# Kernel optimization log

Measured on AMD Instinct MI355X. Metric: run time of the kernel, lower is better.

The kernel has to match this reference:

```python
import jax, jax.numpy as jnp
import numpy as np

EPS = 1e-6
N_LATENT = 64
LITTLE_LATENT = 16
PATCH = 5
N_PATCH_SIDE = 21           # (63+2-5)/3+1
N_PATCHES = N_PATCH_SIDE ** 2  # 441
DEC_SIDE = 13               # decoder fold uses 13x13 = 169 tiles


def _make_patch_kernel():
    # Faithful to create_kernel(): eps-filled kernel with identity taps, grouped per color channel.
    k = np.full((25, 25), EPS, dtype=np.float32)
    k[np.arange(25), np.arange(25)] += 1.0
    k = k.reshape(25, 1, PATCH, PATCH)
    return jnp.asarray(np.tile(k, (3, 1, 1, 1)))  # (75, 1, 5, 5), OIHW


def extract_image_patches(x):
    # x: [B, 3, 63, 63] -> [B, 441, 3, 5, 5]
    kern = _make_patch_kernel().astype(x.dtype)
    out = jax.lax.conv_general_dilated(
        x, kern, window_strides=(3, 3), padding=((1, 1), (1, 1)),
        feature_group_count=3, dimension_numbers=('NCHW', 'OIHW', 'NCHW'))  # [B, 75, 21, 21]
    B = x.shape[0]
    out = out.reshape(B, 3, PATCH, PATCH, N_PATCHES)
    return out.transpose(0, 4, 1, 2, 3)


def little_encode(p_flat, le_w1, le_b1, le_w2, le_b2):
    # p_flat: [N, 75] -> mean, logvar each [N, 16]
    h = jax.nn.relu(p_flat @ le_w1 + le_b1)
    stats = h @ le_w2 + le_b2
    return stats[:, :LITTLE_LATENT], stats[:, LITTLE_LATENT:]


def little_decode(z, ld_w1, ld_b1, ld_w2, ld_b2):
    # z: [N, 16] -> [N, 3, 5, 5]
    h = jax.nn.relu(z @ ld_w1 + ld_b1)
    out = jax.nn.sigmoid(h @ ld_w2 + ld_b2)
    return out.reshape(-1, 3, PATCH, PATCH)


def setup_inputs() -> dict:
    key = jax.random.key(0)
    ks = jax.random.split(key, 20)
    B = 256
    s = 0.02  # weight init scale for numerical sanity
    inp = {
        'x': jax.random.uniform(ks[0], (B, 3, 63, 63), jnp.float32),
        'noise_little': jax.random.normal(ks[1], (B, N_PATCHES, LITTLE_LATENT), jnp.float32),
        'noise_z': jax.random.normal(ks[2], (B, N_LATENT), jnp.float32),
        # little VAE params (LittleVAE_V2([3,5,5],16), MLP stand-in)
        'le_w1': jax.random.normal(ks[3], (75, 128), jnp.float32) * s,
        'le_b1': jnp.zeros((128,), jnp.float32),
        'le_w2': jax.random.normal(ks[4], (128, 2 * LITTLE_LATENT), jnp.float32) * s,
        'le_b2': jnp.zeros((2 * LITTLE_LATENT,), jnp.float32),
        'ld_w1': jax.random.normal(ks[5], (LITTLE_LATENT, 128), jnp.float32) * s,
        'ld_b1': jnp.zeros((128,), jnp.float32),
        'ld_w2': jax.random.normal(ks[6], (128, 75), jnp.float32) * s,
        'ld_b2': jnp.zeros((75,), jnp.float32),
        # encoder_mlp: Linear(7056,4096) ReLU Linear(4096,2*n_latent) ReLU
        'enc_w1': jax.random.normal(ks[7], (7056, 4096), jnp.float32) * s,
        'enc_b1': jnp.zeros((4096,), jnp.float32),
        'enc_w2': jax.random.normal(ks[8], (4096, 2 * N_LATENT), jnp.float32) * s,
        'enc_b2': jnp.zeros((2 * N_LATENT,), jnp.float32),
        # decoder_mlp: Linear(n_latent,32) ReLU Linear(32,4096) ReLU Linear(4096,7056) ReLU
        'dec_w1': jax.random.normal(ks[9], (N_LATENT, 32), jnp.float32) * s,
        'dec_b1': jnp.zeros((32,), jnp.float32),
        'dec_w2': jax.random.normal(ks[10], (32, 4096), jnp.float32) * s,
        'dec_b2': jnp.zeros((4096,), jnp.float32),
        'dec_w3': jax.random.normal(ks[11], (4096, 7056), jnp.float32) * s,
        'dec_b3': jnp.zeros((7056,), jnp.float32),
    }
    return inp


def reference(x, noise_little, noise_z,
              le_w1, le_b1, le_w2, le_b2, ld_w1, ld_b1, ld_w2, ld_b2,
              enc_w1, enc_b1, enc_w2, enc_b2,
              dec_w1, dec_b1, dec_w2, dec_b2, dec_w3, dec_b3):
    B = x.shape[0]
    patches = extract_image_patches(x)                      # [B, 441, 3, 5, 5]
    p_flat = patches.reshape(B * N_PATCHES, 75)
    m_l, lv_l = little_encode(p_flat, le_w1, le_b1, le_w2, le_b2)  # [B*441, 16]
    z_l = noise_little.reshape(B * N_PATCHES, LITTLE_LATENT) * jnp.exp(0.5 * lv_l) + m_l
    next_layer_input = z_l.reshape(B, N_PATCHES, 1, LITTLE_LATENT)

    # hierarchical encode (note trailing ReLU applies to mean/logvar, as in source)
    h = jax.nn.relu(next_layer_input.reshape(B, -1) @ enc_w1 + enc_b1)
    stats = jax.nn.relu(h @ enc_w2 + enc_b2)
    mean, logvar = stats[:, :N_LATENT], stats[:, N_LATENT:]
    z = noise_z * jnp.exp(0.5 * logvar) + mean

    # hierarchical decode
    h = jax.nn.relu(z @ dec_w1 + dec_b1)
    h = jax.nn.relu(h @ dec_w2 + dec_b2)
    latent = jax.nn.relu(h @ dec_w3 + dec_b3).reshape(B, N_PATCHES, 1, LITTLE_LATENT)

    # fold first 169 decoded 5x5 tiles (stride 5 => non-overlapping) into 65x65, crop to 64x64
    z_tiles = latent[:, :DEC_SIDE * DEC_SIDE, 0, :].reshape(B * DEC_SIDE * DEC_SIDE, LITTLE_LATENT)
    tiles = little_decode(z_tiles, ld_w1, ld_b1, ld_w2, ld_b2)  # [B*169, 3, 5, 5]
    tiles = tiles.reshape(B, DEC_SIDE, DEC_SIDE, 3, PATCH, PATCH)
    canvas = tiles.transpose(0, 3, 1, 4, 2, 5).reshape(B, 3, DEC_SIDE * PATCH, DEC_SIDE * PATCH)
    img = canvas[:, :, :-1, :-1]                             # [B, 3, 64, 64]
    return (latent, mean, logvar, next_layer_input, img)
```

## Files before the change

### kernel.cpp

```cpp
#include <hip/hip_runtime.h>
#include <math.h>

#define EPSF 1e-6f

typedef __attribute__((ext_vector_type(8))) short short8v;
typedef __attribute__((ext_vector_type(4))) float f32x4;
typedef __attribute__((ext_vector_type(4))) unsigned short u16x4;

__device__ __forceinline__ unsigned short f2bf(float f) {
    union { float f; unsigned u; } v; v.f = f;
    return (unsigned short)((v.u + 0x7FFFu + ((v.u >> 16) & 1u)) >> 16);
}
__device__ __forceinline__ int swe(int row, int k) {
    return (row << 7) + (k ^ ((row & 7) << 3));
}
__device__ __forceinline__ int swe64(int row, int k) {
    return (row << 6) + (k ^ ((row & 7) << 3));
}

__global__ __launch_bounds__(256) void k_little_encode_mfma(
    const float* __restrict__ x,
    const float* __restrict__ noise,
    const float* __restrict__ w1,
    const float* __restrict__ b1,
    const float* __restrict__ w2,
    const float* __restrict__ b2,
    float* __restrict__ nli,
    unsigned short* __restrict__ nli_bf)
{
    __shared__ __align__(16) unsigned short pS[128 * 128];
    __shared__ __align__(16) unsigned short w1S[128 * 128];
    __shared__ __align__(16) unsigned short hS[128 * 128];
    __shared__ __align__(16) unsigned short w2S[32 * 128];
    __shared__ float b1S[128];
    __shared__ float b2S[32];
    __shared__ float sums[128][4];

    int t = threadIdx.x;

    {
        uint4 z4 = make_uint4(0, 0, 0, 0);
        #pragma unroll
        for (int i = 0; i < 8; ++i) {
            *(uint4*)&pS[(i * 256 + t) * 8]  = z4;
            *(uint4*)&w1S[(i * 256 + t) * 8] = z4;
        }
    }
    __syncthreads();

    for (int k = (t >> 4); k < 75; k += 16) {
        int n0 = (t & 15) * 8;
        float4 a0 = *(const float4*)(w1 + k * 128 + n0);
        float4 a1 = *(const float4*)(w1 + k * 128 + n0 + 4);
        w1S[swe(n0 + 0, k)] = f2bf(a0.x);
        w1S[swe(n0 + 1, k)] = f2bf(a0.y);
        w1S[swe(n0 + 2, k)] = f2bf(a0.z);
        w1S[swe(n0 + 3, k)] = f2bf(a0.w);
        w1S[swe(n0 + 4, k)] = f2bf(a1.x);
        w1S[swe(n0 + 5, k)] = f2bf(a1.y);
        w1S[swe(n0 + 6, k)] = f2bf(a1.z);
        w1S[swe(n0 + 7, k)] = f2bf(a1.w);
    }
    for (int k = (t >> 3); k < 128; k += 32) {
        int n0 = (t & 7) * 4;
        float4 a = *(const float4*)(w2 + k * 32 + n0);
        w2S[swe(n0 + 0, k)] = f2bf(a.x);
        w2S[swe(n0 + 1, k)] = f2bf(a.y);
        w2S[swe(n0 + 2, k)] = f2bf(a.z);
        w2S[swe(n0 + 3, k)] = f2bf(a.w);
    }
    if (t < 128) b1S[t] = b1[t];
    if (t < 32)  b2S[t] = b2[t];

    int row  = t & 127;
    int half = t >> 7;
    int R0 = blockIdx.x * 128 + row;
    int bb = R0 / 441;
    int p  = R0 - bb * 441;
    int pi = p / 21, pj = p - pi * 21;
    const float* xb = x + (size_t)bb * 3 * 63 * 63;

    float v[38];
    {
        float sA = 0.f, sB = 0.f;
        if (half == 0) {
            #pragma unroll
            for (int i = 0; i < 38; ++i) {
                const int k = i;
                const int c = k / 25, o = k % 25, ph = o / 5, pw = o % 5;
                int y = pi * 3 + ph - 1, xx = pj * 3 + pw - 1;
                float val = 0.f;
                if ((unsigned)y < 63u && (unsigned)xx < 63u)
                    val = xb[(c * 63 + y) * 63 + xx];
                v[i] = val;
                if (k < 25) sA += val; else sB += val;
            }
        } else {
            #pragma unroll
            for (int i = 0; i < 37; ++i) {
                const int k = 38 + i;
                const int c = k / 25, o = k % 25, ph = o / 5, pw = o % 5;
                int y = pi * 3 + ph - 1, xx = pj * 3 + pw - 1;
                float val = 0.f;
                if ((unsigned)y < 63u && (unsigned)xx < 63u)
                    val = xb[(c * 63 + y) * 63 + xx];
                v[i] = val;
                if (k < 50) sA += val; else sB += val;
            }
        }
        sums[row][half * 2 + 0] = sA;
        sums[row][half * 2 + 1] = sB;
    }
    __syncthreads();
    {
        float c0 = sums[row][0];
        float c1 = sums[row][1] + sums[row][2];
        float c2 = sums[row][3];
        if (half == 0) {
            #pragma unroll
            for (int i = 0; i < 38; ++i) {
                const int k = i;
                float cs = (k < 25) ? c0 : c1;
                pS[swe(row, k)] = f2bf(v[i] + EPSF * cs);
            }
        } else {
            #pragma unroll
            for (int i = 0; i < 37; ++i) {
                const int k = 38 + i;
                float cs = (k < 50) ? c1 : c2;
                pS[swe(row, k)] = f2bf(v[i] + EPSF * cs);
            }
        }
    }
    __syncthreads();

    int w = t >> 6, lane = t & 63, lr = lane & 15, lg = lane >> 4;

    f32x4 acc[2][8];
    #pragma unroll
    for (int mi = 0; mi < 2; ++mi)
        #pragma unroll
        for (int ni = 0; ni < 8; ++ni)
            acc[mi][ni] = (f32x4){0.f, 0.f, 0.f, 0.f};

    #pragma unroll
    for (int ks = 0; ks < 3; ++ks) {
        int kb = ks * 32 + lg * 8;
        short8v a0 = *(const short8v*)&pS[swe(w * 32 + lr, kb)];
        short8v a1 = *(const short8v*)&pS[swe(w * 32 + 16 + lr, kb)];
        #pragma unroll
        for (int ni = 0; ni < 8; ++ni) {
            short8v bf = *(const short8v*)&w1S[swe(ni * 16 + lr, kb)];
            acc[0][ni] = __builtin_amdgcn_mfma_f32_16x16x32_bf16(a0, bf, acc[0][ni], 0, 0, 0);
            acc[1][ni] = __builtin_amdgcn_mfma_f32_16x16x32_bf16(a1, bf, acc[1][ni], 0, 0, 0);
        }
    }
    #pragma unroll
    for (int mi = 0; mi < 2; ++mi)
        #pragma unroll
        for (int ni = 0; ni < 8; ++ni) {
            int n = ni * 16 + lr;
            float bv = b1S[n];
            #pragma unroll
            for (int r = 0; r < 4; ++r) {
                int m = w * 32 + mi * 16 + lg * 4 + r;
                hS[swe(m, n)] = f2bf(fmaxf(acc[mi][ni][r] + bv, 0.f));
            }
        }

    f32x4 acc2[2][2];
    #pragma unroll
    for (int mi = 0; mi < 2; ++mi)
        #pragma unroll
        for (int ni = 0; ni < 2; ++ni)
            acc2[mi][ni] = (f32x4){0.f, 0.f, 0.f, 0.f};

    #pragma unroll
    for (int kh = 0; kh < 4; ++kh) {
        int kb = kh * 32 + lg * 8;
        short8v a0 = *(const short8v*)&hS[swe(w * 32 + lr, kb)];
        short8v a1 = *(const short8v*)&hS[swe(w * 32 + 16 + lr, kb)];
        #pragma unroll
        for (int ni = 0; ni < 2; ++ni) {
            short8v bf = *(const short8v*)&w2S[swe(ni * 16 + lr, kb)];
            acc2[0][ni] = __builtin_amdgcn_mfma_f32_16x16x32_bf16(a0, bf, acc2[0][ni], 0, 0, 0);
            acc2[1][ni] = __builtin_amdgcn_mfma_f32_16x16x32_bf16(a1, bf, acc2[1][ni], 0, 0, 0);
        }
    }

    #pragma unroll
    for (int mi = 0; mi < 2; ++mi)
        #pragma unroll
        for (int r = 0; r < 4; ++r) {
            int m = w * 32 + mi * 16 + lg * 4 + r;
            size_t R = (size_t)blockIdx.x * 128 + m;
            float mean = acc2[mi][0][r] + b2S[lr];
            float lv   = acc2[mi][1][r] + b2S[16 + lr];
            float z = noise[R * 16 + lr] * expf(0.5f * lv) + mean;
            nli[R * 16 + lr] = z;
            nli_bf[R * 16 + lr] = f2bf(z);
        }
}

__global__ __launch_bounds__(256) void k_little_decode_mfma(
    const float* __restrict__ latent,
    const float* __restrict__ w1,
    const float* __restrict__ b1,
    const float* __restrict__ w2,
    const float* __restrict__ b2,
    float* __restrict__ img)
{
    __shared__ __align__(16) unsigned short w1S[128 * 64];
    __shared__ __align__(16) unsigned short hS[128 * 128];
    __shared__ __align__(16) unsigned short w2S[80 * 128];
    __shared__ float b1S[128];
    __shared__ float b2S[80];

    int t = threadIdx.x;

    {
        uint4 z4 = make_uint4(0, 0, 0, 0);
        #pragma unroll
        for (int i = 0; i < 4; ++i)
            *(uint4*)&w1S[(i * 256 + t) * 8] = z4;
        #pragma unroll
        for (int i = 0; i < 5; ++i)
            *(uint4*)&w2S[(i * 256 + t) * 8] = z4;
    }
    __syncthreads();

    {
        int k = t >> 4;
        int n0 = (t & 15) * 8;
        float4 a0 = *(const float4*)(w1 + k * 128 + n0);
        float4 a1 = *(const float4*)(w1 + k * 128 + n0 + 4);
        w1S[swe64(n0 + 0, k)] = f2bf(a0.x);
        w1S[swe64(n0 + 1, k)] = f2bf(a0.y);
        w1S[swe64(n0 + 2, k)] = f2bf(a0.z);
        w1S[swe64(n0 + 3, k)] = f2bf(a0.w);
        w1S[swe64(n0 + 4, k)] = f2bf(a1.x);
        w1S[swe64(n0 + 5, k)] = f2bf(a1.y);
        w1S[swe64(n0 + 6, k)] = f2bf(a1.z);
        w1S[swe64(n0 + 7, k)] = f2bf(a1.w);
    }
    {
        int k = t >> 1;
        int half = t & 1;
        int n0 = half ? 38 : 0, n1 = half ? 75 : 38;
        for (int n = n0; n < n1; ++n)
            w2S[swe(n, k)] = f2bf(w2[k * 75 + n]);
    }
    if (t < 128) b1S[t] = b1[t];
    if (t < 80)  b2S[t] = (t < 75) ? b2[t] : 0.f;
    __syncthreads();

    int w = t >> 6, lane = t & 63, lr = lane & 15, lg = lane >> 4;

    f32x4 acc[2][8];
    #pragma unroll
    for (int mi = 0; mi < 2; ++mi)
        #pragma unroll
        for (int ni = 0; ni < 8; ++ni)
            acc[mi][ni] = (f32x4){0.f, 0.f, 0.f, 0.f};

    short8v af[2];
    #pragma unroll
    for (int mi = 0; mi < 2; ++mi) {
        int m = w * 32 + mi * 16 + lr;
        int R = blockIdx.x * 128 + m;
        int b = R / 169, tt = R - 169 * b;
        if (lg < 2) {
            const float* zp = latent + (size_t)b * 7056 + tt * 16 + lg * 8;
            float4 f0 = *(const float4*)(zp);
            float4 f1 = *(const float4*)(zp + 4);
            af[mi][0] = (short)f2bf(f0.x); af[mi][1] = (short)f2bf(f0.y);
            af[mi][2] = (short)f2bf(f0.z); af[mi][3] = (short)f2bf(f0.w);
            af[mi][4] = (short)f2bf(f1.x); af[mi][5] = (short)f2bf(f1.y);
            af[mi][6] = (short)f2bf(f1.z); af[mi][7] = (short)f2bf(f1.w);
        } else {
            af[mi] = (short8v){0,0,0,0,0,0,0,0};
        }
    }
    {
        int kb = lg * 8;
        #pragma unroll
        for (int ni = 0; ni < 8; ++ni) {
            short8v bf = *(const short8v*)&w1S[swe64(ni * 16 + lr, kb)];
            acc[0][ni] = __builtin_amdgcn_mfma_f32_16x16x32_bf16(af[0], bf, acc[0][ni], 0, 0, 0);
            acc[1][ni] = __builtin_amdgcn_mfma_f32_16x16x32_bf16(af[1], bf, acc[1][ni], 0, 0, 0);
        }
    }
    #pragma unroll
    for (int mi = 0; mi < 2; ++mi)
        #pragma unroll
        for (int ni = 0; ni < 8; ++ni) {
            int n = ni * 16 + lr;
            float bv = b1S[n];
            #pragma unroll
            for (int r = 0; r < 4; ++r) {
                int m = w * 32 + mi * 16 + lg * 4 + r;
                hS[swe(m, n)] = f2bf(fmaxf(acc[mi][ni][r] + bv, 0.f));
            }
        }

    f32x4 acc2[2][5];
    #pragma unroll
    for (int mi = 0; mi < 2; ++mi)
        #pragma unroll
        for (int ni = 0; ni < 5; ++ni)
            acc2[mi][ni] = (f32x4){0.f, 0.f, 0.f, 0.f};

    #pragma unroll
    for (int kh = 0; kh < 4; ++kh) {
        int kb = kh * 32 + lg * 8;
        short8v a0 = *(const short8v*)&hS[swe(w * 32 + lr, kb)];
        short8v a1 = *(const short8v*)&hS[swe(w * 32 + 16 + lr, kb)];
        #pragma unroll
        for (int ni = 0; ni < 5; ++ni) {
            short8v bf = *(const short8v*)&w2S[swe(ni * 16 + lr, kb)];
            acc2[0][ni] = __builtin_amdgcn_mfma_f32_16x16x32_bf16(a0, bf, acc2[0][ni], 0, 0, 0);
            acc2[1][ni] = __builtin_amdgcn_mfma_f32_16x16x32_bf16(a1, bf, acc2[1][ni], 0, 0, 0);
        }
    }

    #pragma unroll
    for (int mi = 0; mi < 2; ++mi)
        #pragma unroll
        for (int r = 0; r < 4; ++r) {
            int m = w * 32 + mi * 16 + lg * 4 + r;
            int R = blockIdx.x * 128 + m;
            int b = R / 169, tt = R - 169 * b;
            int ti = tt / 13, tj = tt - 13 * ti;
            #pragma unroll
            for (int ni = 0; ni < 5; ++ni) {
                int col = ni * 16 + lr;
                if (col < 75) {
                    float a = acc2[mi][ni][r] + b2S[col];
                    float o = 1.f / (1.f + expf(-a));
                    int c = col / 25, o25 = col - 25 * c;
                    int ph = o25 / 5, pw = o25 - 5 * ph;
                    int y = ti * 5 + ph, xx = tj * 5 + pw;
                    if (y < 64 && xx < 64)
                        img[(((size_t)b * 3 + c) * 64 + y) * 64 + xx] = o;
                }
            }
        }
}

template<int EPI>
__global__ __launch_bounds__(512, 2) void k_gemm_pipe(
    const unsigned short* __restrict__ A,
    const float* __restrict__ W,
    float* __restrict__ C,
    int N, int K, int baseSteps)
{
    __shared__ __align__(16) unsigned short As[2][256 * 64];
    __shared__ __align__(16) unsigned short Ws[2][128 * 64];

    int t = threadIdx.x;
    int bn = blockIdx.x * 128;
    int totalSteps = (K + 63) >> 6;
    int step0 = blockIdx.y * baseSteps;
    int nSteps = totalSteps - step0;
    if (nSteps > baseSteps) nSteps = baseSteps;
    if (nSteps <= 0) return;
    const bool nfull = (bn + 128 <= N);

    int w = t >> 6, lane = t & 63, lr = lane & 15, lg = lane >> 4;
    int wr = w >> 1, wc = w & 1;

    int ar = t >> 1, ah = (t & 1) * 32;
    const unsigned short* Arow = A + (size_t)ar * K + ah;

    int nq = t & 31, kb = (t >> 5) * 4;
    int nc = bn + 4 * nq;

    uint4  aP[4];
    float4 wP[4];

    f32x4 acc[4][4];
    #pragma unroll
    for (int i = 0; i < 4; ++i)
        #pragma unroll
        for (int j = 0; j < 4; ++j)
            acc[i][j] = (f32x4){0.f, 0.f, 0.f, 0.f};

    #define LOAD_T(stepIdx)                                                   \
    do {                                                                      \
        int kk0 = (stepIdx) << 6;                                             \
        if ((kk0 + 64 <= K) && nfull) {                                       \
            const uint4* ap = (const uint4*)(Arow + kk0);                     \
            _Pragma("unroll")                                                 \
            for (int u = 0; u < 4; ++u) aP[u] = ap[u];                        \
            const float* wp = W + (size_t)(kk0 + kb) * N + nc;                \
            _Pragma("unroll")                                                 \
            for (int jj = 0; jj < 4; ++jj)                                    \
                wP[jj] = *(const float4*)(wp + (size_t)jj * N);               \
        } else {                                                              \
            _Pragma("unroll")                                                 \
            for (int u = 0; u < 4; ++u) {                                     \
                int ak = kk0 + ah + u * 8;                                    \
                if (ak + 8 <= K) aP[u] = *(const uint4*)(Arow + kk0 + u * 8); \
                else             aP[u] = make_uint4(0, 0, 0, 0);              \
            }                                                                 \
            _Pragma("unroll")                                                 \
            for (int jj = 0; jj < 4; ++jj) {                                  \
                int kr = kk0 + kb + jj;                                       \
                float4 tmp = {0.f, 0.f, 0.f, 0.f};                            \
                if (kr < K) {                                                 \
                    const float* wp = W + (size_t)kr * N;                     \
                    if (nfull) tmp = *(const float4*)(wp + nc);               \
                    else {                                                    \
                        tmp.x = (nc + 0 < N) ? wp[nc + 0] : 0.f;              \
                        tmp.y = (nc + 1 < N) ? wp[nc + 1] : 0.f;              \
                        tmp.z = (nc + 2 < N) ? wp[nc + 2] : 0.f;              \
                        tmp.w = (nc + 3 < N) ? wp[nc + 3] : 0.f;              \
                    }                                                         \
                }                                                             \
                wP[jj] = tmp;                                                 \
            }                                                                 \
        }                                                                     \
    } while (0)

    #define STORE_T(buf)                                                      \
    do {                                                                      \
        _Pragma("unroll")                                                     \
        for (int u = 0; u < 4; ++u)                                           \
            *(uint4*)&As[buf][swe64(ar, ah + u * 8)] = aP[u];                 \
        _Pragma("unroll")                                                     \
        for (int c4 = 0; c4 < 4; ++c4) {                                      \
            int n = 4 * nq + c4;                                              \
            float e0 = (c4 == 0) ? wP[0].x : (c4 == 1) ? wP[0].y              \
                     : (c4 == 2) ? wP[0].z : wP[0].w;                         \
            float e1 = (c4 == 0) ? wP[1].x : (c4 == 1) ? wP[1].y              \
                     : (c4 == 2) ? wP[1].z : wP[1].w;                         \
            float e2 = (c4 == 0) ? wP[2].x : (c4 == 1) ? wP[2].y              \
                     : (c4 == 2) ? wP[2].z : wP[2].w;                         \
            float e3 = (c4 == 0) ? wP[3].x : (c4 == 1) ? wP[3].y              \
                     : (c4 == 2) ? wP[3].z : wP[3].w;                         \
            u16x4 pk;                                                         \
            pk.x = f2bf(e0); pk.y = f2bf(e1);                                 \
            pk.z = f2bf(e2); pk.w = f2bf(e3);                                 \
            *(u16x4*)&Ws[buf][swe64(n, kb)] = pk;                             \
        }                                                                     \
    } while (0)

    #define MFMA_T(buf)                                                       \
    do {                                                                      \
        _Pragma("unroll")                                                     \
        for (int kk = 0; kk < 64; kk += 32) {                                 \
            int kbase = kk + lg * 8;                                          \
            short8v afr[4], bfr[4];                                           \
            _Pragma("unroll")                                                 \
            for (int mi = 0; mi < 4; ++mi)                                    \
                afr[mi] = *(const short8v*)&As[buf][                          \
                    swe64(wr * 64 + mi * 16 + lr, kbase)];                    \
            _Pragma("unroll")                                                 \
            for (int ni = 0; ni < 4; ++ni)                                    \
                bfr[ni] = *(const short8v*)&Ws[buf][                          \
                    swe64(wc * 64 + ni * 16 + lr, kbase)];                    \
            _Pragma("unroll")                                                 \
            for (int mi = 0; mi < 4; ++mi)                                    \
                _Pragma("unroll")                                             \
                for (int ni = 0; ni < 4; ++ni)                                \
                    acc[mi][ni] = __builtin_amdgcn_mfma_f32_16x16x32_bf16(    \
                        afr[mi], bfr[ni], acc[mi][ni], 0, 0, 0);              \
        }                                                                     \
    } while (0)

    #define FENCE_BAR                                                         \
    do {                                                                      \
        asm volatile("s_waitcnt lgkmcnt(0)" ::: "memory");                    \
        __builtin_amdgcn_s_barrier();                                         \
        __builtin_amdgcn_sched_barrier(0);                                    \
    } while (0)

    LOAD_T(step0);
    STORE_T(0);
    if (nSteps > 1) LOAD_T(step0 + 1);
    FENCE_BAR;

    int cur = 0;
    for (int ti = 0; ti < nSteps; ++ti) {
        if (ti + 1 < nSteps) {
            STORE_T(cur ^ 1);
            if (ti + 2 < nSteps) LOAD_T(step0 + ti + 2);
        }
        __builtin_amdgcn_s_setprio(1);
        MFMA_T(cur);
        __builtin_amdgcn_s_setprio(0);
        FENCE_BAR;
        cur ^= 1;
    }
    #undef LOAD_T
    #undef STORE_T
    #undef MFMA_T
    #undef FENCE_BAR

    if (EPI == 1) {
        float* Cz = C + (size_t)blockIdx.y * 256 * N;
        #pragma unroll
        for (int ni = 0; ni < 4; ++ni) {
            int col = bn + wc * 64 + ni * 16 + lr;
            if (col < N) {
                #pragma unroll
                for (int mi = 0; mi < 4; ++mi) {
                    int row = wr * 64 + mi * 16 + lg * 4;
                    #pragma unroll
                    for (int r = 0; r < 4; ++r)
                        Cz[(size_t)(row + r) * N + col] = acc[mi][ni][r];
                }
            }
        }
    } else {
        #pragma unroll
        for (int ni = 0; ni < 4; ++ni) {
            int col = bn + wc * 64 + ni * 16 + lr;
            if (col < N) {
                #pragma unroll
                for (int mi = 0; mi < 4; ++mi) {
                    int row = wr * 64 + mi * 16 + lg * 4;
                    #pragma unroll
                    for (int r = 0; r < 4; ++r)
                        __hip_atomic_fetch_add(&C[(size_t)(row + r) * N + col],
                                               acc[mi][ni][r],
                                               __ATOMIC_RELAXED,
                                               __HIP_MEMORY_SCOPE_AGENT);
                }
            }
        }
    }
}

__global__ __launch_bounds__(256) void k_reduce_bias_relu(
    const float* __restrict__ parts, const float* __restrict__ bias,
    float* __restrict__ out, int S, int N)
{
    int nF4 = (256 / 4) * N;
    int nCol4 = N >> 2;
    size_t strideF4 = (size_t)64 * N;
    for (int idx = blockIdx.x * 256 + threadIdx.x; idx < nF4;
         idx += gridDim.x * 256) {
        int col4 = idx % nCol4;
        float4 b = *(const float4*)(bias + col4 * 4);
        float4 a = ((const float4*)parts)[idx];
        for (int z = 1; z < S; ++z) {
            float4 p = ((const float4*)parts)[(size_t)z * strideF4 + idx];
            a.x += p.x; a.y += p.y; a.z += p.z; a.w += p.w;
        }
        a.x = fmaxf(a.x + b.x, 0.f);
        a.y = fmaxf(a.y + b.y, 0.f);
        a.z = fmaxf(a.z + b.z, 0.f);
        a.w = fmaxf(a.w + b.w, 0.f);
        ((float4*)out)[idx] = a;
    }
}

__global__ __launch_bounds__(256) void k_stats_partial(
    const float* __restrict__ h_e,
    const float* __restrict__ w2,
    float* __restrict__ psum)
{
    __shared__ float hs[16][256];
    int mg = blockIdx.x >> 4;
    int ks = blockIdx.x & 15;
    int t = threadIdx.x;

    for (int i = t; i < 16 * 256; i += 256) {
        int mm = i >> 8, kk = i & 255;
        hs[mm][kk] = h_e[(size_t)(mg * 16 + mm) * 4096 + ks * 256 + kk];
    }
    __syncthreads();

    int n = t & 127, mh = t >> 7;
    float acc[8] = {0.f,0.f,0.f,0.f,0.f,0.f,0.f,0.f};
    const float* w2p = w2 + (size_t)(ks * 256) * 128 + n;
    for (int k = 0; k < 256; ++k) {
        float wv = w2p[(size_t)k * 128];
        #pragma unroll
        for (int mm = 0; mm < 8; ++mm)
            acc[mm] += hs[mh * 8 + mm][k] * wv;
    }
    #pragma unroll
    for (int mm = 0; mm < 8; ++mm) {
        int m = mg * 16 + mh * 8 + mm;
        psum[((size_t)m * 16 + ks) * 128 + n] = acc[mm];
    }
}

__global__ __launch_bounds__(256) void k_mid2(
    const float* __restrict__ psum,
    const float* __restrict__ enc_b2,
    const float* __restrict__ noise_z,
    const float* __restrict__ dec_w1, const float* __restrict__ dec_b1,
    const float* __restrict__ dec_w2, const float* __restrict__ dec_b2,
    float* __restrict__ mean_out, float* __restrict__ logvar_out,
    unsigned short* __restrict__ h2bf)
{
    __shared__ float st[128];
    __shared__ float z_s[64];
    __shared__ float h1_s[32];

    int m = blockIdx.x >> 2, ch = blockIdx.x & 3;
    int t = threadIdx.x;

    if (t < 128) {
        float a = enc_b2[t];
        #pragma unroll 4
        for (int ks = 0; ks < 16; ++ks)
            a += psum[((size_t)m * 16 + ks) * 128 + t];
        st[t] = fmaxf(a, 0.f);
    }
    __syncthreads();

    if (t < 64) {
        float mean = st[t], lv = st[t + 64];
        if (ch == 0) {
            mean_out[(size_t)m * 64 + t]   = mean;
            logvar_out[(size_t)m * 64 + t] = lv;
        }
        z_s[t] = noise_z[(size_t)m * 64 + t] * expf(0.5f * lv) + mean;
    }
    __syncthreads();

    if (t < 32) {
        float a = dec_b1[t];
        #pragma unroll 8
        for (int k = 0; k < 64; ++k) a += z_s[k] * dec_w1[k * 32 + t];
        h1_s[t] = fmaxf(a, 0.f);
    }
    __syncthreads();

    #pragma unroll
    for (int j = 0; j < 4; ++j) {
        int nn = ch * 1024 + j * 256 + t;
        float a = dec_b2[nn];
        #pragma unroll 8
        for (int k = 0; k < 32; ++k)
            a += h1_s[k] * dec_w2[(size_t)k * 4096 + nn];
        h2bf[(size_t)m * 4096 + nn] = f2bf(fmaxf(a, 0.f));
    }
}

extern "C" void kernel_launch(void* const* d_in, const int* in_sizes, int n_in,
                              void* d_out, int out_size, void* d_ws, size_t ws_size,
                              hipStream_t stream) {
    const float* x            = (const float*)d_in[0];
    const float* noise_little = (const float*)d_in[1];
    const float* noise_z      = (const float*)d_in[2];
    const float* le_w1        = (const float*)d_in[3];
    const float* le_b1        = (const float*)d_in[4];
    const float* le_w2        = (const float*)d_in[5];
    const float* le_b2        = (const float*)d_in[6];
    const float* ld_w1        = (const float*)d_in[7];
    const float* ld_b1        = (const float*)d_in[8];
    const float* ld_w2        = (const float*)d_in[9];
    const float* ld_b2        = (const float*)d_in[10];
    const float* enc_w1       = (const float*)d_in[11];
    const float* enc_b1       = (const float*)d_in[12];
    const float* enc_w2       = (const float*)d_in[13];
    const float* enc_b2       = (const float*)d_in[14];
    const float* dec_w1       = (const float*)d_in[15];
    const float* dec_b1       = (const float*)d_in[16];
    const float* dec_w2       = (const float*)d_in[17];
    const float* dec_b2       = (const float*)d_in[18];
    const float* dec_w3       = (const float*)d_in[19];
    const float* dec_b3       = (const float*)d_in[20];

    float* out = (float*)d_out;
    float* latent = out;
    float* mean   = latent + 1806336;
    float* logvar = mean + 16384;
    float* nli    = logvar + 16384;
    float* img    = nli + 1806336;

    float* h_e = latent;

    unsigned short* nli_bf = (unsigned short*)d_ws;
    float* psum = (float*)((char*)d_ws + 3612672);
    unsigned short* h2bf = (unsigned short*)((char*)d_ws + 5709824);
    float* parts = (float*)((char*)d_ws + 7806976);

    const size_t base = 7806976;
    const size_t slice1 = (size_t)256 * 4096 * 4;
    const size_t slice2 = (size_t)256 * 7056 * 4;
    int S1 = (ws_size > base) ? (int)((ws_size - base) / slice1) : 0;
    int S2 = (ws_size > base) ? (int)((ws_size - base) / slice2) : 0;
    if (S1 > 8) S1 = 8;
    if (S2 > 8) S2 = 8;
    if (S1 < 4) S1 = 0;
    if (S2 < 4) S2 = 0;


    k_little_encode_mfma<<<882, 256, 0, stream>>>(
        x, noise_little, le_w1, le_b1, le_w2, le_b2, nli, nli_bf);

    if (S1) {
        int bs = (111 + S1 - 1) / S1;
        k_gemm_pipe<1><<<dim3(32, S1), 512, 0, stream>>>(
            nli_bf, enc_w1, parts, 4096, 7056, bs);
        k_reduce_bias_relu<<<1024, 256, 0, stream>>>(
            parts, enc_b1, h_e, S1, 4096);
    } else {
        hipMemsetAsync(h_e, 0, (size_t)256 * 4096 * 4, stream);
        k_gemm_pipe<0><<<dim3(32, 8), 512, 0, stream>>>(
            nli_bf, enc_w1, h_e, 4096, 7056, 14);
        k_reduce_bias_relu<<<1024, 256, 0, stream>>>(
            h_e, enc_b1, h_e, 1, 4096);
    }

    k_stats_partial<<<256, 256, 0, stream>>>(h_e, enc_w2, psum);
    k_mid2<<<1024, 256, 0, stream>>>(
        psum, enc_b2, noise_z, dec_w1, dec_b1, dec_w2, dec_b2,
        mean, logvar, h2bf);

    if (S2) {
        int bs = (64 + S2 - 1) / S2;
        k_gemm_pipe<1><<<dim3(56, S2), 512, 0, stream>>>(
            h2bf, dec_w3, parts, 7056, 4096, bs);
        k_reduce_bias_relu<<<1764, 256, 0, stream>>>(
            parts, dec_b3, latent, S2, 7056);
    } else {
        hipMemsetAsync(latent, 0, (size_t)1806336 * 4, stream);
        k_gemm_pipe<0><<<dim3(56, 4), 512, 0, stream>>>(
            h2bf, dec_w3, latent, 7056, 4096, 16);
        k_reduce_bias_relu<<<1764, 256, 0, stream>>>(
            latent, dec_b3, latent, 1, 7056);
    }

    k_little_decode_mfma<<<338, 256, 0, stream>>>(
        latent, ld_w1, ld_b1, ld_w2, ld_b2, img);
}
```

Before: 201.7 us.

## Split GEMM M-dimension across blocks, register double-buffer, fuse reduce into stats

The pipelined bf16 GEMM now uses 256-thread blocks covering 128 rows, with the M split moved into grid.y and the K split into grid.z. Each thread loads 8 W rows per step into two alternating register buffers, prefetching two steps ahead, and W is stored to LDS as 8-wide vectors with a new swizzle. The encoder bias+ReLU reduction kernel is removed; k_stats_partial now sums the split-K partials, adds the bias and applies ReLU itself. This saves one launch and one pass over h_e. The split counts are now fixed (8 and 4) instead of derived from workspace size, and register pressure rises from the doubled prefetch buffers.

```diff
diff --git a/kernel.cpp b/kernel.cpp
--- a/kernel.cpp
+++ b/kernel.cpp
@@ -4,6 +4,7 @@
 #define EPSF 1e-6f
 
 typedef __attribute__((ext_vector_type(8))) short short8v;
+typedef __attribute__((ext_vector_type(8))) unsigned short u16x8;
 typedef __attribute__((ext_vector_type(4))) float f32x4;
 typedef __attribute__((ext_vector_type(4))) unsigned short u16x4;
 
@@ -16,6 +17,10 @@
 }
 __device__ __forceinline__ int swe64(int row, int k) {
     return (row << 6) + (k ^ ((row & 7) << 3));
+}
+__device__ __forceinline__ int swn(int n, int k) {
+    return (n << 6) + (k & 7) +
+           ((((k >> 3) & 7) ^ ((n + (n >> 2)) & 7)) << 3);
 }
 
 __global__ __launch_bounds__(256) void k_little_encode_mfma(
@@ -348,19 +353,20 @@
 }
 
 template<int EPI>
-__global__ __launch_bounds__(512, 2) void k_gemm_pipe(
+__global__ __launch_bounds__(256, 2) void k_gemm_pipe(
     const unsigned short* __restrict__ A,
     const float* __restrict__ W,
     float* __restrict__ C,
     int N, int K, int baseSteps)
 {
-    __shared__ __align__(16) unsigned short As[2][256 * 64];
+    __shared__ __align__(16) unsigned short As[2][128 * 64];
     __shared__ __align__(16) unsigned short Ws[2][128 * 64];
 
     int t = threadIdx.x;
     int bn = blockIdx.x * 128;
+    int m0 = blockIdx.y * 128;
     int totalSteps = (K + 63) >> 6;
-    int step0 = blockIdx.y * baseSteps;
+    int step0 = blockIdx.z * baseSteps;
     int nSteps = totalSteps - step0;
     if (nSteps > baseSteps) nSteps = baseSteps;
     if (nSteps <= 0) return;
@@ -370,13 +376,13 @@
     int wr = w >> 1, wc = w & 1;
 
     int ar = t >> 1, ah = (t & 1) * 32;
-    const unsigned short* Arow = A + (size_t)ar * K + ah;
-
-    int nq = t & 31, kb = (t >> 5) * 4;
+    const unsigned short* Arow = A + (size_t)(m0 + ar) * K + ah;
+
+    int nq = t & 31, kb = (t >> 5) * 8;
     int nc = bn + 4 * nq;
 
-    uint4  aP[4];
-    float4 wP[4];
+    uint4  aPa[4], aPb[4];
+    float4 wPa[8], wPb[8];
 
     f32x4 acc[4][4];
     #pragma unroll
@@ -385,26 +391,26 @@
         for (int j = 0; j < 4; ++j)
             acc[i][j] = (f32x4){0.f, 0.f, 0.f, 0.f};
 
-    #define LOAD_T(stepIdx)                                                   \
+    #define LOAD_T(AP, WP, stepIdx)                                           \
     do {                                                                      \
         int kk0 = (stepIdx) << 6;                                             \
         if ((kk0 + 64 <= K) && nfull) {                                       \
             const uint4* ap = (const uint4*)(Arow + kk0);                     \
             _Pragma("unroll")                                                 \
-            for (int u = 0; u < 4; ++u) aP[u] = ap[u];                        \
+            for (int u = 0; u < 4; ++u) AP[u] = ap[u];                        \
             const float* wp = W + (size_t)(kk0 + kb) * N + nc;                \
             _Pragma("unroll")                                                 \
-            for (int jj = 0; jj < 4; ++jj)                                    \
-                wP[jj] = *(const float4*)(wp + (size_t)jj * N);               \
+            for (int jj = 0; jj < 8; ++jj)                                    \
+                WP[jj] = *(const float4*)(wp + (size_t)jj * N);               \
         } else {                                                              \
             _Pragma("unroll")                                                 \
             for (int u = 0; u < 4; ++u) {                                     \
                 int ak = kk0 + ah + u * 8;                                    \
-                if (ak + 8 <= K) aP[u] = *(const uint4*)(Arow + kk0 + u * 8); \
-                else             aP[u] = make_uint4(0, 0, 0, 0);              \
+                if (ak + 8 <= K) AP[u] = *(const uint4*)(Arow + kk0 + u * 8); \
+                else             AP[u] = make_uint4(0, 0, 0, 0);              \
             }                                                                 \
             _Pragma("unroll")                                                 \
-            for (int jj = 0; jj < 4; ++jj) {                                  \
+            for (int jj = 0; jj < 8; ++jj) {                                  \
                 int kr = kk0 + kb + jj;                                       \
                 float4 tmp = {0.f, 0.f, 0.f, 0.f};                            \
                 if (kr < K) {                                                 \
@@ -417,31 +423,27 @@
                         tmp.w = (nc + 3 < N) ? wp[nc + 3] : 0.f;              \
                     }                                                         \
                 }                                                             \
-                wP[jj] = tmp;                                                 \
+                WP[jj] = tmp;                                                 \
             }                                                                 \
         }                                                                     \
     } while (0)
 
-    #define STORE_T(buf)                                                      \
+    #define STORE_T(buf, AP, WP)                                              \
     do {                                                                      \
         _Pragma("unroll")                                                     \
         for (int u = 0; u < 4; ++u)                                           \
-            *(uint4*)&As[buf][swe64(ar, ah + u * 8)] = aP[u];                 \
+            *(uint4*)&As[buf][swe64(ar, ah + u * 8)] = AP[u];                 \
         _Pragma("unroll")                                                     \
         for (int c4 = 0; c4 < 4; ++c4) {                                      \
             int n = 4 * nq + c4;                                              \
-            float e0 = (c4 == 0) ? wP[0].x : (c4 == 1) ? wP[0].y              \
-                     : (c4 == 2) ? wP[0].z : wP[0].w;                         \
-            float e1 = (c4 == 0) ? wP[1].x : (c4 == 1) ? wP[1].y              \
-                     : (c4 == 2) ? wP[1].z : wP[1].w;                         \
-            float e2 = (c4 == 0) ? wP[2].x : (c4 == 1) ? wP[2].y              \
-                     : (c4 == 2) ? wP[2].z : wP[2].w;                         \
-            float e3 = (c4 == 0) ? wP[3].x : (c4 == 1) ? wP[3].y              \
-                     : (c4 == 2) ? wP[3].z : wP[3].w;                         \
-            u16x4 pk;                                                         \
-            pk.x = f2bf(e0); pk.y = f2bf(e1);                                 \
-            pk.z = f2bf(e2); pk.w = f2bf(e3);                                 \
-            *(u16x4*)&Ws[buf][swe64(n, kb)] = pk;                             \
+            u16x8 pk;                                                         \
+            _Pragma("unroll")                                                 \
+            for (int jj = 0; jj < 8; ++jj) {                                  \
+                float e = (c4 == 0) ? WP[jj].x : (c4 == 1) ? WP[jj].y         \
+                        : (c4 == 2) ? WP[jj].z : WP[jj].w;                    \
+                pk[jj] = f2bf(e);                                             \
+            }                                                                 \
+            *(u16x8*)&Ws[buf][swn(n, kb)] = pk;                               \
         }                                                                     \
     } while (0)
 
@@ -458,7 +460,7 @@
             _Pragma("unroll")                                                 \
             for (int ni = 0; ni < 4; ++ni)                                    \
                 bfr[ni] = *(const short8v*)&Ws[buf][                          \
-                    swe64(wc * 64 + ni * 16 + lr, kbase)];                    \
+                    swn(wc * 64 + ni * 16 + lr, kbase)];                      \
             _Pragma("unroll")                                                 \
             for (int mi = 0; mi < 4; ++mi)                                    \
                 _Pragma("unroll")                                             \
@@ -475,22 +477,30 @@
         __builtin_amdgcn_sched_barrier(0);                                    \
     } while (0)
 
-    LOAD_T(step0);
-    STORE_T(0);
-    if (nSteps > 1) LOAD_T(step0 + 1);
+    LOAD_T(aPa, wPa, step0);
+    if (nSteps > 1) LOAD_T(aPb, wPb, step0 + 1);
+    STORE_T(0, aPa, wPa);
+    if (nSteps > 2) LOAD_T(aPa, wPa, step0 + 2);
     FENCE_BAR;
 
-    int cur = 0;
-    for (int ti = 0; ti < nSteps; ++ti) {
+    for (int ti = 0; ti < nSteps; ti += 2) {
         if (ti + 1 < nSteps) {
-            STORE_T(cur ^ 1);
-            if (ti + 2 < nSteps) LOAD_T(step0 + ti + 2);
+            STORE_T(1, aPb, wPb);
+            if (ti + 3 < nSteps) LOAD_T(aPb, wPb, step0 + ti + 3);
         }
         __builtin_amdgcn_s_setprio(1);
-        MFMA_T(cur);
+        MFMA_T(0);
         __builtin_amdgcn_s_setprio(0);
         FENCE_BAR;
-        cur ^= 1;
+        if (ti + 1 >= nSteps) break;
+        if (ti + 2 < nSteps) {
+            STORE_T(0, aPa, wPa);
+            if (ti + 4 < nSteps) LOAD_T(aPa, wPa, step0 + ti + 4);
+        }
+        __builtin_amdgcn_s_setprio(1);
+        MFMA_T(1);
+        __builtin_amdgcn_s_setprio(0);
+        FENCE_BAR;
     }
     #undef LOAD_T
     #undef STORE_T
@@ -498,14 +508,14 @@
     #undef FENCE_BAR
 
     if (EPI == 1) {
-        float* Cz = C + (size_t)blockIdx.y * 256 * N;
+        float* Cz = C + (size_t)blockIdx.z * 256 * N;
         #pragma unroll
         for (int ni = 0; ni < 4; ++ni) {
             int col = bn + wc * 64 + ni * 16 + lr;
             if (col < N) {
                 #pragma unroll
                 for (int mi = 0; mi < 4; ++mi) {
-                    int row = wr * 64 + mi * 16 + lg * 4;
+                    int row = m0 + wr * 64 + mi * 16 + lg * 4;
                     #pragma unroll
                     for (int r = 0; r < 4; ++r)
                         Cz[(size_t)(row + r) * N + col] = acc[mi][ni][r];
@@ -519,7 +529,7 @@
             if (col < N) {
                 #pragma unroll
                 for (int mi = 0; mi < 4; ++mi) {
-                    int row = wr * 64 + mi * 16 + lg * 4;
+                    int row = m0 + wr * 64 + mi * 16 + lg * 4;
                     #pragma unroll
                     for (int r = 0; r < 4; ++r)
                         __hip_atomic_fetch_add(&C[(size_t)(row + r) * N + col],
@@ -557,9 +567,11 @@
 }
 
 __global__ __launch_bounds__(256) void k_stats_partial(
-    const float* __restrict__ h_e,
+    const float* __restrict__ parts,
+    const float* __restrict__ enc_b1,
     const float* __restrict__ w2,
-    float* __restrict__ psum)
+    float* __restrict__ psum,
+    int S)
 {
     __shared__ float hs[16][256];
     int mg = blockIdx.x >> 4;
@@ -568,7 +580,11 @@
 
     for (int i = t; i < 16 * 256; i += 256) {
         int mm = i >> 8, kk = i & 255;
-        hs[mm][kk] = h_e[(size_t)(mg * 16 + mm) * 4096 + ks * 256 + kk];
+        size_t off = (size_t)(mg * 16 + mm) * 4096 + ks * 256 + kk;
+        float v = enc_b1[ks * 256 + kk];
+        for (int z = 0; z < S; ++z)
+            v += parts[(size_t)z * 1048576 + off];
+        hs[mm][kk] = fmaxf(v, 0.f);
     }
     __syncthreads();
 
@@ -684,45 +700,35 @@
     const size_t base = 7806976;
     const size_t slice1 = (size_t)256 * 4096 * 4;
     const size_t slice2 = (size_t)256 * 7056 * 4;
-    int S1 = (ws_size > base) ? (int)((ws_size - base) / slice1) : 0;
-    int S2 = (ws_size > base) ? (int)((ws_size - base) / slice2) : 0;
-    if (S1 > 8) S1 = 8;
-    if (S2 > 8) S2 = 8;
-    if (S1 < 4) S1 = 0;
-    if (S2 < 4) S2 = 0;
-
+    const int S1 = (ws_size >= base + 8 * slice1) ? 8 : 0;
+    const int S2 = (ws_size >= base + 4 * slice2) ? 4 : 0;
 
     k_little_encode_mfma<<<882, 256, 0, stream>>>(
         x, noise_little, le_w1, le_b1, le_w2, le_b2, nli, nli_bf);
 
     if (S1) {
-        int bs = (111 + S1 - 1) / S1;
-        k_gemm_pipe<1><<<dim3(32, S1), 512, 0, stream>>>(
-            nli_bf, enc_w1, parts, 4096, 7056, bs);
-        k_reduce_bias_relu<<<1024, 256, 0, stream>>>(
-            parts, enc_b1, h_e, S1, 4096);
+        k_gemm_pipe<1><<<dim3(32, 2, 8), 256, 0, stream>>>(
+            nli_bf, enc_w1, parts, 4096, 7056, 14);
+        k_stats_partial<<<256, 256, 0, stream>>>(parts, enc_b1, enc_w2, psum, 8);
     } else {
-        hipMemsetAsync(h_e, 0, (size_t)256 * 4096 * 4, stream);
-        k_gemm_pipe<0><<<dim3(32, 8), 512, 0, stream>>>(
+        hipMemsetAsync(h_e, 0, slice1, stream);
+        k_gemm_pipe<0><<<dim3(32, 2, 8), 256, 0, stream>>>(
             nli_bf, enc_w1, h_e, 4096, 7056, 14);
-        k_reduce_bias_relu<<<1024, 256, 0, stream>>>(
-            h_e, enc_b1, h_e, 1, 4096);
-    }
-
-    k_stats_partial<<<256, 256, 0, stream>>>(h_e, enc_w2, psum);
+        k_stats_partial<<<256, 256, 0, stream>>>(h_e, enc_b1, enc_w2, psum, 1);
+    }
+
     k_mid2<<<1024, 256, 0, stream>>>(
         psum, enc_b2, noise_z, dec_w1, dec_b1, dec_w2, dec_b2,
         mean, logvar, h2bf);
 
     if (S2) {
-        int bs = (64 + S2 - 1) / S2;
-        k_gemm_pipe<1><<<dim3(56, S2), 512, 0, stream>>>(
-            h2bf, dec_w3, parts, 7056, 4096, bs);
+        k_gemm_pipe<1><<<dim3(56, 2, 4), 256, 0, stream>>>(
+            h2bf, dec_w3, parts, 7056, 4096, 16);
         k_reduce_bias_relu<<<1764, 256, 0, stream>>>(
-            parts, dec_b3, latent, S2, 7056);
+            parts, dec_b3, latent, 4, 7056);
     } else {
-        hipMemsetAsync(latent, 0, (size_t)1806336 * 4, stream);
-        k_gemm_pipe<0><<<dim3(56, 4), 512, 0, stream>>>(
+        hipMemsetAsync(latent, 0, slice2, stream);
+        k_gemm_pipe<0><<<dim3(56, 2, 4), 256, 0, stream>>>(
             h2bf, dec_w3, latent, 7056, 4096, 16);
         k_reduce_bias_relu<<<1764, 256, 0, stream>>>(
             latent, dec_b3, latent, 1, 7056);
```

Measured after the change: 232.3 us. 1.15x slower.
